# Performance work log

Measured on AMD Instinct MI355X. Metric: run time of the kernel, lower is better.

The kernel has to match this reference:

```python
import jax, jax.numpy as jnp
import numpy as np

CE_SLICES = [(1,10),(12,29),(30,33),(33,40),(40,64),(64,79),(79,84),(84,94),(94,96),(96,99),(99,105),(105,113),(116,122),(122,128),(128,151),(151,159),(160,165)]
MSE_COLS = [0,10,11,29,113,114,115,159,165,166,167]
BINS = 800
RATIO_JSD = 0.1  # stand-in for par.RATIO_JSD (not defined in source)
B = 262144


def setup_inputs() -> dict:
    key = jax.random.key(0)
    k1, k2, k3, k4 = jax.random.split(key, 4)
    data_encoded = jax.random.normal(k1, (B, 11), dtype=jnp.float32)
    data_decoded = jax.random.normal(k2, (B, 168), dtype=jnp.float32)
    data_true = jax.random.normal(k3, (B, 168), dtype=jnp.float32)
    # categorical blocks of data_true must be one-hot (nonzero-based decode)
    for j, (s, e) in enumerate(CE_SLICES):
        lab = jax.random.randint(jax.random.fold_in(k3, j), (B,), 0, e - s)
        data_true = data_true.at[:, s:e].set(jax.nn.one_hot(lab, e - s, dtype=jnp.float32))
    label_true = jax.random.randint(k4, (B, 1), 0, 2).astype(jnp.float32)
    return {"data_encoded": data_encoded, "data_decoded": data_decoded,
            "data_true": data_true, "label_true": label_true, "batch_size": B}


def _ce(logits, labels):
    # F.cross_entropy with mean reduction
    logp = jax.nn.log_softmax(logits, axis=-1)
    return -jnp.mean(jnp.take_along_axis(logp, labels[:, None], axis=1))


def _hist(x, mn, mx, mask):
    # torch.histc semantics: BINS equal bins on [mn, mx], top edge inclusive.
    t = (x - mn) / (mx - mn)
    idx = jnp.clip(jnp.floor(t * BINS).astype(jnp.int32), 0, BINS - 1)
    return jax.ops.segment_sum(mask, idx, num_segments=BINS)


def _kl(p, q, eps=1e-12):
    return jnp.sum(jnp.where(p > 0, p * jnp.log((p + eps) / (q + eps)), 0.0))


def reference(data_encoded, data_decoded, data_true, label_true, batch_size):
    # ---- MSE losses over 11 scalar columns (vectorized) ----
    cols = jnp.array(MSE_COLS)
    diff = data_decoded[:, cols] - data_true[:, cols]            # [B, 11]
    mse_loss = jnp.sum(jnp.mean(diff * diff, axis=0))

    # ---- 17 cross-entropy heads (labels decoded from one-hot blocks) ----
    ce_loss = jnp.float32(0.0)
    for s, e in CE_SLICES:
        labels = jnp.argmax(data_true[:, s:e], axis=1)           # == first nonzero for one-hot
        ce_loss = ce_loss + _ce(data_decoded[:, s:e], labels)

    # ---- JSD between male/female histograms of first 10 encoded dims ----
    combined = jnp.concatenate([data_encoded, label_true], axis=1)  # [B, 12]
    mn = jnp.min(combined, axis=0)
    mx = jnp.max(combined, axis=0)
    male = (combined[:, 11] == 0).astype(jnp.float32)
    female = (combined[:, 11] == 1).astype(jnp.float32)
    cols10 = combined[:, :10].T                                  # [10, B]
    hist = jax.vmap(_hist, in_axes=(0, 0, 0, None))              # [10, BINS]
    m_h = hist(cols10, mn[:10], mx[:10], male) / jnp.sum(male)
    f_h = hist(cols10, mn[:10], mx[:10], female) / jnp.sum(female)
    mid = 0.5 * (m_h + f_h)
    kld = 0.5 * (_kl(m_h, mid) + _kl(f_h, mid))                  # Jensen-Shannon divergence

    multi = (1.0 - RATIO_JSD) * (mse_loss + ce_loss) + RATIO_JSD * kld
    return jnp.stack([multi, mse_loss, ce_loss, RATIO_JSD * kld])
```

## Files before the change

kernel.cpp:

```cpp
#include <hip/hip_runtime.h>
#include <math.h>


#define BINS 800
#define NHCOLS 10
#define HB 64

#define MIN_OFF 0
#define MAX_OFF 16
#define CNT_OFF 32
#define SUM_OFF 34
#define MH_OFF  64
#define FH_OFF  8064
#define PART_OFF 16384
#define WS_INIT_U32 64

__device__ __forceinline__ unsigned f2ord(float f) {
  unsigned u = __float_as_uint(f);
  return (u & 0x80000000u) ? ~u : (u | 0x80000000u);
}
__device__ __forceinline__ float ord2f(unsigned e) {
  return __uint_as_float((e & 0x80000000u) ? (e & 0x7FFFFFFFu) : ~e);
}

__global__ void k_init(unsigned* __restrict__ ws) {
  int i = blockIdx.x * blockDim.x + threadIdx.x;
  if (i < WS_INIT_U32) ws[i] = (i < 11) ? 0xFFFFFFFFu : 0u;
}

__global__ __launch_bounds__(256) void k_minmax(const float* __restrict__ enc,
                                                const float* __restrict__ lab,
                                                unsigned* __restrict__ ws, int B) {
  const int tid    = blockIdx.x * blockDim.x + threadIdx.x;
  const int stride = gridDim.x * blockDim.x;
  const int c      = tid % 11;
  unsigned mn = 0xFFFFFFFFu, mx = 0u;
  const long long total = (long long)B * 11;
  for (long long i = tid; i < total; i += stride) {
    unsigned e = f2ord(enc[i]);
    mn = mn < e ? mn : e;
    mx = mx > e ? mx : e;
  }
  __shared__ unsigned smn[11], smx[11], scnt[2];
  if (threadIdx.x < 11) { smn[threadIdx.x] = 0xFFFFFFFFu; smx[threadIdx.x] = 0u; }
  if (threadIdx.x < 2)  scnt[threadIdx.x] = 0u;
  __syncthreads();
  atomicMin(&smn[c], mn);
  atomicMax(&smx[c], mx);
  unsigned m = 0, f = 0;
  for (int i = tid; i < B; i += stride) {
    float v = lab[i];
    m += (v == 0.0f);
    f += (v == 1.0f);
  }
  atomicAdd(&scnt[0], m);
  atomicAdd(&scnt[1], f);
  __syncthreads();
  if (threadIdx.x < 11) {
    atomicMin(&ws[MIN_OFF + threadIdx.x], smn[threadIdx.x]);
    atomicMax(&ws[MAX_OFF + threadIdx.x], smx[threadIdx.x]);
  }
  if (threadIdx.x == 11) atomicAdd(&ws[CNT_OFF + 0], scnt[0]);
  if (threadIdx.x == 12) atomicAdd(&ws[CNT_OFF + 1], scnt[1]);
}

__global__ __launch_bounds__(256) void k_hist(const float* __restrict__ enc,
                                              const float* __restrict__ lab,
                                              unsigned* __restrict__ ws, int B) {
  __shared__ unsigned h[2][NHCOLS * BINS];
  unsigned* hf = &h[0][0];
  for (int i = threadIdx.x; i < 2 * NHCOLS * BINS; i += blockDim.x) hf[i] = 0u;
  float mn[NHCOLS], rng[NHCOLS];
#pragma unroll
  for (int c = 0; c < NHCOLS; ++c) {
    float lo = ord2f(ws[MIN_OFF + c]);
    float hi = ord2f(ws[MAX_OFF + c]);
    mn[c] = lo; rng[c] = hi - lo;
  }
  __syncthreads();
  const int sub = (threadIdx.x >> 6) & 1;
  for (int r = blockIdx.x * 256 + threadIdx.x; r < B; r += HB * 256) {
    float lv = lab[r];
    unsigned add = (lv == 0.0f) ? 1u : ((lv == 1.0f) ? 0x10000u : 0u);
    if (add) {
      const float* row = enc + (long long)r * 11;
#pragma unroll
      for (int c = 0; c < NHCOLS; ++c) {
        float t = (row[c] - mn[c]) / rng[c];
        int b = (int)floorf(t * 800.0f);
        b = b < 0 ? 0 : (b > BINS - 1 ? BINS - 1 : b);
        atomicAdd(&h[sub][c * BINS + b], add);
      }
    }
  }
  __syncthreads();
  for (int i = threadIdx.x; i < NHCOLS * BINS; i += blockDim.x)
    ws[PART_OFF + blockIdx.x * (NHCOLS * BINS) + i] = h[0][i] + h[1][i];
}

__global__ __launch_bounds__(256) void k_merge(unsigned* __restrict__ ws) {
  int i = blockIdx.x * blockDim.x + threadIdx.x;
  if (i >= NHCOLS * BINS) return;
  unsigned m = 0, f = 0;
  for (int p = 0; p < HB; ++p) {
    unsigned v = ws[PART_OFF + p * (NHCOLS * BINS) + i];
    m += v & 0xFFFFu;
    f += v >> 16;
  }
  ws[MH_OFF + i] = m;
  ws[FH_OFF + i] = f;
}

__host__ __device__ constexpr int slice_of(int c) {
  return (c>=1&&c<10)?0:(c>=12&&c<29)?1:(c>=30&&c<33)?2:(c>=33&&c<40)?3:
         (c>=40&&c<64)?4:(c>=64&&c<79)?5:(c>=79&&c<84)?6:(c>=84&&c<94)?7:
         (c>=94&&c<96)?8:(c>=96&&c<99)?9:(c>=99&&c<105)?10:(c>=105&&c<113)?11:
         (c>=116&&c<122)?12:(c>=122&&c<128)?13:(c>=128&&c<151)?14:
         (c>=151&&c<159)?15:(c>=160&&c<165)?16:-1;
}
__host__ __device__ constexpr bool mse_of(int c) {
  return c==0||c==10||c==11||c==29||c==113||c==114||c==115||c==159||
         c==165||c==166||c==167;
}

template<int I, int K>
__device__ __forceinline__ void elem(const float (&d)[11][4], const float (&t)[11][4],
                                     float (&s)[17], float &dot, float &mse, int j) {
  constexpr int c0 = 16*I + K, c1 = c0+4, c2 = c0+8, c3 = c0+12;
  constexpr int cem = ((c0<168 && slice_of(c0)>=0)?1:0) |
                      ((c1<168 && slice_of(c1)>=0)?2:0) |
                      ((c2<168 && slice_of(c2)>=0)?4:0) |
                      ((c3<168 && slice_of(c3)>=0)?8:0);
  constexpr int msm = ((c0<168 && mse_of(c0))?1:0) | ((c1<168 && mse_of(c1))?2:0) |
                      ((c2<168 && mse_of(c2))?4:0) | ((c3<168 && mse_of(c3))?8:0);
  const float dv = d[I][K], tv = t[I][K];
  if constexpr (cem != 0) {
    float e = __expf(dv);
    if constexpr (cem & 1) s[slice_of(c0)] += (j == 0) ? e : 0.0f;
    if constexpr (cem & 2) s[slice_of(c1)] += (j == 1) ? e : 0.0f;
    if constexpr (cem & 4) s[slice_of(c2)] += (j == 2) ? e : 0.0f;
    if constexpr (cem & 8) s[slice_of(c3)] += (j == 3) ? e : 0.0f;
    dot += ((cem >> j) & 1) ? tv * dv : 0.0f;
  }
  if constexpr (msm != 0) {
    float df = dv - tv;
    mse += ((msm >> j) & 1) ? df * df : 0.0f;
  }
}

template<int I>
__device__ __forceinline__ void elem_row(const float (&d)[11][4], const float (&t)[11][4],
                                         float (&s)[17], float &dot, float &mse, int j) {
  elem<I,0>(d, t, s, dot, mse, j);
  elem<I,1>(d, t, s, dot, mse, j);
  elem<I,2>(d, t, s, dot, mse, j);
  elem<I,3>(d, t, s, dot, mse, j);
}

__global__ __launch_bounds__(256) void k_main(const float* __restrict__ dec,
                                              const float* __restrict__ tru,
                                              float* __restrict__ wsf, int B) {
  const int lane = threadIdx.x & 63;
  const int wid  = threadIdx.x >> 6;
  const int j    = lane & 3;
  const int row  = blockIdx.x * 64 + (wid << 4) + (lane >> 2);
  const bool valid = row < B;

  float d[11][4], t[11][4];
  const float4* d4 = (const float4*)(dec + (size_t)row * 168);
  const float4* t4 = (const float4*)(tru + (size_t)row * 168);
#pragma unroll
  for (int i = 0; i < 11; ++i) {
    const int w = 4 * i + j;
    float4 dv = make_float4(0.f, 0.f, 0.f, 0.f);
    float4 tv = make_float4(0.f, 0.f, 0.f, 0.f);
    if (valid && w < 42) { dv = d4[w]; tv = t4[w]; }
    d[i][0] = dv.x; d[i][1] = dv.y; d[i][2] = dv.z; d[i][3] = dv.w;
    t[i][0] = tv.x; t[i][1] = tv.y; t[i][2] = tv.z; t[i][3] = tv.w;
  }

  float s[17];
#pragma unroll
  for (int k = 0; k < 17; ++k) s[k] = 0.0f;
  float dot = 0.0f, mse = 0.0f;

  elem_row<0>(d, t, s, dot, mse, j);
  elem_row<1>(d, t, s, dot, mse, j);
  elem_row<2>(d, t, s, dot, mse, j);
  elem_row<3>(d, t, s, dot, mse, j);
  elem_row<4>(d, t, s, dot, mse, j);
  elem_row<5>(d, t, s, dot, mse, j);
  elem_row<6>(d, t, s, dot, mse, j);
  elem_row<7>(d, t, s, dot, mse, j);
  elem_row<8>(d, t, s, dot, mse, j);
  elem_row<9>(d, t, s, dot, mse, j);
  elem_row<10>(d, t, s, dot, mse, j);

  dot += __shfl_xor(dot, 1, 64);
  dot += __shfl_xor(dot, 2, 64);
#pragma unroll
  for (int k = 0; k < 17; ++k) {
    s[k] += __shfl_xor(s[k], 1, 64);
    s[k] += __shfl_xor(s[k], 2, 64);
  }
  float ce = -dot;
#pragma unroll
  for (int k = 0; k < 17; ++k) ce += __logf(s[k]);

  ce  = (valid && j == 0) ? ce : 0.0f;
  mse = valid ? mse : 0.0f;

  __shared__ float sm[4], sc[4];
#pragma unroll
  for (int off = 32; off > 0; off >>= 1) {
    mse += __shfl_down(mse, off, 64);
    ce  += __shfl_down(ce, off, 64);
  }
  if (lane == 0) { sm[wid] = mse; sc[wid] = ce; }
  __syncthreads();
  if (threadIdx.x == 0) {
    atomicAdd(&wsf[SUM_OFF + 0], sm[0] + sm[1] + sm[2] + sm[3]);
    atomicAdd(&wsf[SUM_OFF + 1], sc[0] + sc[1] + sc[2] + sc[3]);
  }
}

__global__ __launch_bounds__(256) void k_final(const unsigned* __restrict__ ws,
                                               float* __restrict__ out, int B) {
  const float* wsf = (const float*)ws;
  float male   = (float)ws[CNT_OFF + 0];
  float female = (float)ws[CNT_OFF + 1];
  float local = 0.0f;
  for (int i = threadIdx.x; i < NHCOLS * BINS; i += blockDim.x) {
    float mh  = (float)ws[MH_OFF + i] / male;
    float fh  = (float)ws[FH_OFF + i] / female;
    float mid = 0.5f * (mh + fh);
    if (mh > 0.0f) local += mh * logf((mh + 1e-12f) / (mid + 1e-12f));
    if (fh > 0.0f) local += fh * logf((fh + 1e-12f) / (mid + 1e-12f));
  }
  __shared__ float s[4];
  int lane = threadIdx.x & 63, wid = threadIdx.x >> 6;
#pragma unroll
  for (int off = 32; off > 0; off >>= 1) local += __shfl_down(local, off, 64);
  if (lane == 0) s[wid] = local;
  __syncthreads();
  if (threadIdx.x == 0) {
    float kld   = 0.5f * (s[0] + s[1] + s[2] + s[3]);
    float mse   = wsf[SUM_OFF + 0] / (float)B;
    float ce    = wsf[SUM_OFF + 1] / (float)B;
    float multi = 0.9f * (mse + ce) + 0.1f * kld;
    out[0] = multi;
    out[1] = mse;
    out[2] = ce;
    out[3] = 0.1f * kld;
  }
}

extern "C" void kernel_launch(void* const* d_in, const int* in_sizes, int n_in,
                              void* d_out, int out_size, void* d_ws, size_t ws_size,
                              hipStream_t stream) {
  (void)n_in; (void)out_size; (void)ws_size;
  const float* enc = (const float*)d_in[0];
  const float* dec = (const float*)d_in[1];
  const float* tru = (const float*)d_in[2];
  const float* lab = (const float*)d_in[3];
  const int B = in_sizes[3];
  unsigned* ws = (unsigned*)d_ws;
  float* out = (float*)d_out;

  hipLaunchKernelGGL(k_init, dim3(1), dim3(64), 0, stream, ws);
  hipLaunchKernelGGL(k_minmax, dim3(352), dim3(256), 0, stream, enc, lab, ws, B);
  hipLaunchKernelGGL(k_hist, dim3(HB), dim3(256), 0, stream, enc, lab, ws, B);
  hipLaunchKernelGGL(k_merge, dim3((NHCOLS * BINS + 255) / 256), dim3(256), 0, stream, ws);
  hipLaunchKernelGGL(k_main, dim3((B + 63) / 64), dim3(256), 0, stream,
                     dec, tru, (float*)ws, B);
  hipLaunchKernelGGL(k_final, dim3(1), dim3(256), 0, stream, ws, out, B);
}
```

Before: 446.6 us.

## Fuse histogram into main loss kernel with global atomics, drop init/merge kernels

Removes the separate init, histogram and merge kernels. Per-block min/max/count partials are now written to workspace and reduced by a single small block. Histogram binning moves into the main decoded/true pass, with each 4-lane group splitting the 10 encoded columns and doing global atomicAdd into male/female bins. This cuts launches and the 64-block shared-memory histogram stage. The cost is heavy contention from global atomics on only 8000 bins, and the histogram zeroing now relies on the partial kernel running first.

Result: slower. 586.3 us (+31.3%).

```diff
diff --git a/kernel.cpp b/kernel.cpp
--- a/kernel.cpp
+++ b/kernel.cpp
@@ -4,7 +4,7 @@
 
 #define BINS 800
 #define NHCOLS 10
-#define HB 64
+#define PB 352
 
 #define MIN_OFF 0
 #define MAX_OFF 16
@@ -13,7 +13,6 @@
 #define MH_OFF  64
 #define FH_OFF  8064
 #define PART_OFF 16384
-#define WS_INIT_U32 64
 
 __device__ __forceinline__ unsigned f2ord(float f) {
   unsigned u = __float_as_uint(f);
@@ -23,17 +22,14 @@
   return __uint_as_float((e & 0x80000000u) ? (e & 0x7FFFFFFFu) : ~e);
 }
 
-__global__ void k_init(unsigned* __restrict__ ws) {
-  int i = blockIdx.x * blockDim.x + threadIdx.x;
-  if (i < WS_INIT_U32) ws[i] = (i < 11) ? 0xFFFFFFFFu : 0u;
-}
-
-__global__ __launch_bounds__(256) void k_minmax(const float* __restrict__ enc,
-                                                const float* __restrict__ lab,
-                                                unsigned* __restrict__ ws, int B) {
-  const int tid    = blockIdx.x * blockDim.x + threadIdx.x;
-  const int stride = gridDim.x * blockDim.x;
-  const int c      = tid % 11;
+__global__ __launch_bounds__(256) void k_part(const float* __restrict__ enc,
+                                              const float* __restrict__ lab,
+                                              unsigned* __restrict__ ws, int B) {
+  const int tid    = blockIdx.x * 256 + threadIdx.x;
+  const int stride = PB * 256;
+  if (tid < 2) ws[SUM_OFF + tid] = 0u;
+  for (int i = tid; i < 2 * BINS * NHCOLS; i += stride) ws[MH_OFF + i] = 0u;
+  const int c = tid % 11;
   unsigned mn = 0xFFFFFFFFu, mx = 0u;
   const long long total = (long long)B * 11;
   for (long long i = tid; i < total; i += stride) {
@@ -41,74 +37,50 @@
     mn = mn < e ? mn : e;
     mx = mx > e ? mx : e;
   }
-  __shared__ unsigned smn[11], smx[11], scnt[2];
-  if (threadIdx.x < 11) { smn[threadIdx.x] = 0xFFFFFFFFu; smx[threadIdx.x] = 0u; }
-  if (threadIdx.x < 2)  scnt[threadIdx.x] = 0u;
-  __syncthreads();
-  atomicMin(&smn[c], mn);
-  atomicMax(&smx[c], mx);
   unsigned m = 0, f = 0;
   for (int i = tid; i < B; i += stride) {
     float v = lab[i];
     m += (v == 0.0f);
     f += (v == 1.0f);
   }
+  __shared__ unsigned smn[11], smx[11], scnt[2];
+  if (threadIdx.x < 11) { smn[threadIdx.x] = 0xFFFFFFFFu; smx[threadIdx.x] = 0u; }
+  if (threadIdx.x < 2)  scnt[threadIdx.x] = 0u;
+  __syncthreads();
+  atomicMin(&smn[c], mn);
+  atomicMax(&smx[c], mx);
   atomicAdd(&scnt[0], m);
   atomicAdd(&scnt[1], f);
   __syncthreads();
+  unsigned* rec = ws + PART_OFF + blockIdx.x * 24;
   if (threadIdx.x < 11) {
-    atomicMin(&ws[MIN_OFF + threadIdx.x], smn[threadIdx.x]);
-    atomicMax(&ws[MAX_OFF + threadIdx.x], smx[threadIdx.x]);
-  }
-  if (threadIdx.x == 11) atomicAdd(&ws[CNT_OFF + 0], scnt[0]);
-  if (threadIdx.x == 12) atomicAdd(&ws[CNT_OFF + 1], scnt[1]);
-}
-
-__global__ __launch_bounds__(256) void k_hist(const float* __restrict__ enc,
-                                              const float* __restrict__ lab,
-                                              unsigned* __restrict__ ws, int B) {
-  __shared__ unsigned h[2][NHCOLS * BINS];
-  unsigned* hf = &h[0][0];
-  for (int i = threadIdx.x; i < 2 * NHCOLS * BINS; i += blockDim.x) hf[i] = 0u;
-  float mn[NHCOLS], rng[NHCOLS];
-#pragma unroll
-  for (int c = 0; c < NHCOLS; ++c) {
-    float lo = ord2f(ws[MIN_OFF + c]);
-    float hi = ord2f(ws[MAX_OFF + c]);
-    mn[c] = lo; rng[c] = hi - lo;
-  }
-  __syncthreads();
-  const int sub = (threadIdx.x >> 6) & 1;
-  for (int r = blockIdx.x * 256 + threadIdx.x; r < B; r += HB * 256) {
-    float lv = lab[r];
-    unsigned add = (lv == 0.0f) ? 1u : ((lv == 1.0f) ? 0x10000u : 0u);
-    if (add) {
-      const float* row = enc + (long long)r * 11;
-#pragma unroll
-      for (int c = 0; c < NHCOLS; ++c) {
-        float t = (row[c] - mn[c]) / rng[c];
-        int b = (int)floorf(t * 800.0f);
-        b = b < 0 ? 0 : (b > BINS - 1 ? BINS - 1 : b);
-        atomicAdd(&h[sub][c * BINS + b], add);
-      }
+    rec[threadIdx.x]      = smn[threadIdx.x];
+    rec[11 + threadIdx.x] = smx[threadIdx.x];
+  }
+  if (threadIdx.x < 2) rec[22 + threadIdx.x] = scnt[threadIdx.x];
+}
+
+__global__ __launch_bounds__(384) void k_reduce(unsigned* __restrict__ ws) {
+  __shared__ unsigned smn[11], smx[11], scnt[2];
+  if (threadIdx.x < 11) { smn[threadIdx.x] = 0xFFFFFFFFu; smx[threadIdx.x] = 0u; }
+  if (threadIdx.x < 2)  scnt[threadIdx.x] = 0u;
+  __syncthreads();
+  for (int p = threadIdx.x; p < PB; p += blockDim.x) {
+    const unsigned* rec = ws + PART_OFF + p * 24;
+#pragma unroll
+    for (int c = 0; c < 11; ++c) {
+      atomicMin(&smn[c], rec[c]);
+      atomicMax(&smx[c], rec[11 + c]);
     }
-  }
-  __syncthreads();
-  for (int i = threadIdx.x; i < NHCOLS * BINS; i += blockDim.x)
-    ws[PART_OFF + blockIdx.x * (NHCOLS * BINS) + i] = h[0][i] + h[1][i];
-}
-
-__global__ __launch_bounds__(256) void k_merge(unsigned* __restrict__ ws) {
-  int i = blockIdx.x * blockDim.x + threadIdx.x;
-  if (i >= NHCOLS * BINS) return;
-  unsigned m = 0, f = 0;
-  for (int p = 0; p < HB; ++p) {
-    unsigned v = ws[PART_OFF + p * (NHCOLS * BINS) + i];
-    m += v & 0xFFFFu;
-    f += v >> 16;
-  }
-  ws[MH_OFF + i] = m;
-  ws[FH_OFF + i] = f;
+    atomicAdd(&scnt[0], rec[22]);
+    atomicAdd(&scnt[1], rec[23]);
+  }
+  __syncthreads();
+  if (threadIdx.x < 11) {
+    ws[MIN_OFF + threadIdx.x] = smn[threadIdx.x];
+    ws[MAX_OFF + threadIdx.x] = smx[threadIdx.x];
+  }
+  if (threadIdx.x < 2) ws[CNT_OFF + threadIdx.x] = scnt[threadIdx.x];
 }
 
 __host__ __device__ constexpr int slice_of(int c) {
@@ -157,9 +129,12 @@
   elem<I,3>(d, t, s, dot, mse, j);
 }
 
-__global__ __launch_bounds__(256) void k_main(const float* __restrict__ dec,
-                                              const float* __restrict__ tru,
-                                              float* __restrict__ wsf, int B) {
+__global__ __launch_bounds__(256) void k_fused(const float* __restrict__ dec,
+                                               const float* __restrict__ tru,
+                                               const float* __restrict__ enc,
+                                               const float* __restrict__ lab,
+                                               unsigned* __restrict__ ws, int B) {
+  float* wsf = (float*)ws;
   const int lane = threadIdx.x & 63;
   const int wid  = threadIdx.x >> 6;
   const int j    = lane & 3;
@@ -177,6 +152,28 @@
     if (valid && w < 42) { dv = d4[w]; tv = t4[w]; }
     d[i][0] = dv.x; d[i][1] = dv.y; d[i][2] = dv.z; d[i][3] = dv.w;
     t[i][0] = tv.x; t[i][1] = tv.y; t[i][2] = tv.z; t[i][3] = tv.w;
+  }
+
+  {
+    const int c0 = (j < 2) ? 3 * j : (6 + 2 * (j - 2));
+    const int nc = (j < 2) ? 3 : 2;
+    float lv = valid ? lab[row] : -1.0f;
+    unsigned base = (lv == 0.0f) ? MH_OFF : ((lv == 1.0f) ? FH_OFF : 0u);
+    if (base) {
+#pragma unroll
+      for (int k = 0; k < 3; ++k) {
+        if (k < nc) {
+          int c = c0 + k;
+          float mnv = ord2f(ws[MIN_OFF + c]);
+          float mxv = ord2f(ws[MAX_OFF + c]);
+          float x = enc[(size_t)row * 11 + c];
+          float tt = (x - mnv) / (mxv - mnv);
+          int b = (int)floorf(tt * 800.0f);
+          b = b < 0 ? 0 : (b > BINS - 1 ? BINS - 1 : b);
+          atomicAdd(&ws[base + c * BINS + b], 1u);
+        }
+      }
+    }
   }
 
   float s[17];
@@ -267,11 +264,9 @@
   unsigned* ws = (unsigned*)d_ws;
   float* out = (float*)d_out;
 
-  hipLaunchKernelGGL(k_init, dim3(1), dim3(64), 0, stream, ws);
-  hipLaunchKernelGGL(k_minmax, dim3(352), dim3(256), 0, stream, enc, lab, ws, B);
-  hipLaunchKernelGGL(k_hist, dim3(HB), dim3(256), 0, stream, enc, lab, ws, B);
-  hipLaunchKernelGGL(k_merge, dim3((NHCOLS * BINS + 255) / 256), dim3(256), 0, stream, ws);
-  hipLaunchKernelGGL(k_main, dim3((B + 63) / 64), dim3(256), 0, stream,
-                     dec, tru, (float*)ws, B);
+  hipLaunchKernelGGL(k_part, dim3(PB), dim3(256), 0, stream, enc, lab, ws, B);
+  hipLaunchKernelGGL(k_reduce, dim3(1), dim3(384), 0, stream, ws);
+  hipLaunchKernelGGL(k_fused, dim3((B + 63) / 64), dim3(256), 0, stream,
+                     dec, tru, enc, lab, ws, B);
   hipLaunchKernelGGL(k_final, dim3(1), dim3(256), 0, stream, ws, out, B);
 }
```
